# Kernel tuning notes

Hardware: AMD Instinct MI355X
Metric: run time of the kernel (lower is better)

The kernel has to match this reference:

```python
import jax, jax.numpy as jnp
import numpy as np

# ---- static config (matches init_kwargs and NSA hyperparams in source) ----
DIM = 512; HEADS = 8; DH = DIM // HEADS; DEPTH = 2
HH = 28; WW = 28; SEQ = HH * WW            # 784
WIN = 28 * 7                                # sliding window = 196
CBS = 28 * 14; CST = 28 * 7                 # compress block 392, stride 196
SBS = 28 * 14; NSEL = 1                     # selection block 392, top-1
NC = (SEQ - CBS) // CST + 1                 # 3 compressed blocks
NS = SEQ // SBS                             # 2 selection blocks
EPS = 1e-5
BATCH = 8


def _overlap_matrix():
    # fraction of each compressed block overlapping each selection block
    O = np.zeros((NC, NS), np.float32)
    for i in range(NC):
        a, b = i * CST, i * CST + CBS
        for j in range(NS):
            c, d = j * SBS, (j + 1) * SBS
            O[i, j] = max(0, min(b, d) - max(a, c)) / CBS
    return jnp.asarray(O)

OVERLAP = _overlap_matrix()  # [NC, NS]


def setup_inputs() -> dict:
    key = jax.random.key(0)
    ks = jax.random.split(key, 12)
    p = lambda i, shape, s=0.02: (jax.random.normal(ks[i], shape, jnp.float32) * s)
    return {
        "x": jax.random.normal(ks[0], (BATCH, DIM, HH, WW), jnp.float32),
        "pos_emb": jax.random.normal(ks[1], (SEQ,), jnp.float32),
        "attn_norm_g": jnp.ones((DEPTH, DIM), jnp.float32),
        "Wq": p(2, (DEPTH, DIM, HEADS * DH)),
        "Wk": p(3, (DEPTH, DIM, HEADS * DH)),
        "Wv": p(4, (DEPTH, DIM, HEADS * DH)),
        "Wo": p(5, (DEPTH, HEADS * DH, DIM)),
        "Wg": p(6, (DEPTH, DIM, HEADS * 3)),
        "ff_norm_g": jnp.ones((DEPTH, DIM), jnp.float32),
        "ff_norm_b": jnp.zeros((DEPTH, DIM), jnp.float32),
        "ff_w1": p(7, (DEPTH, 4 * DIM, DIM)),
        "ff_b1": jnp.zeros((DEPTH, 4 * DIM), jnp.float32),
        "ff_w2": p(8, (DEPTH, DIM, 4 * DIM)),
        "ff_b2": jnp.zeros((DEPTH, DIM), jnp.float32),
    }


def _sparse_attn(x, g, wq, wk, wv, wo, wg):
    # x: [b, n, d]  -- NSA: sliding window + compressed + top-k block selection
    b, n, d = x.shape
    xr = x * jax.lax.rsqrt(jnp.mean(x * x, -1, keepdims=True) + EPS) * g  # RMSNorm
    q = (xr @ wq).reshape(b, n, HEADS, DH)
    k = (xr @ wk).reshape(b, n, HEADS, DH)
    v = (xr @ wv).reshape(b, n, HEADS, DH)
    scale = DH ** -0.5

    # ---- compressed branch: mean-pool overlapping blocks ----
    ck = jnp.stack([k[:, i * CST:i * CST + CBS].mean(1) for i in range(NC)], 1)  # [b,NC,h,dh]
    cv = jnp.stack([v[:, i * CST:i * CST + CBS].mean(1) for i in range(NC)], 1)
    sc = jnp.einsum('bihd,bjhd->bhij', q, ck) * scale          # [b,h,n,NC]
    pc = jax.nn.softmax(sc, -1)
    out_c = jnp.einsum('bhij,bjhd->bihd', pc, cv)              # [b,n,h,dh]

    # ---- selection branch: importance -> top-k selection blocks -> fine attn ----
    imp = jnp.einsum('bhij,jk->bhik', pc, OVERLAP)             # [b,h,n,NS]
    _, sel = jax.lax.top_k(imp, NSEL)                          # [b,h,n,NSEL]
    selmask = jax.nn.one_hot(sel, NS, dtype=jnp.float32).sum(-2) > 0  # [b,h,n,NS]
    blk = jnp.arange(n) // SBS                                 # token -> selection block
    tokmask = selmask[..., blk]                                # [b,h,n,n]
    sf = jnp.einsum('bihd,bjhd->bhij', q, k) * scale           # full fine scores (shared)
    neg = jnp.finfo(sf.dtype).min
    ps = jax.nn.softmax(jnp.where(tokmask, sf, neg), -1)
    out_s = jnp.einsum('bhij,bjhd->bihd', ps, v)

    # ---- sliding window branch ----
    idx = jnp.arange(n)
    winmask = jnp.abs(idx[:, None] - idx[None, :]) < WIN       # [n,n]
    pw = jax.nn.softmax(jnp.where(winmask, sf, neg), -1)
    out_w = jnp.einsum('bhij,bjhd->bihd', pw, v)

    # ---- per-head learned gates over the 3 branches ----
    gates = jax.nn.sigmoid(xr @ wg).reshape(b, n, HEADS, 3)
    o = (gates[..., 0:1] * out_c + gates[..., 1:2] * out_s + gates[..., 2:3] * out_w)
    return o.reshape(b, n, HEADS * DH) @ wo


def _ff(x, g, bb, w1, b1, w2, b2):
    # x: [b,c,h,w]; LayerNorm over channel dim, then 1x1 conv -> GELU -> 1x1 conv
    mean = x.mean(1, keepdims=True)
    var = jnp.var(x, 1, keepdims=True)
    xn = (x - mean) / jnp.sqrt(var + EPS) * g[None, :, None, None] + bb[None, :, None, None]
    h1 = jax.nn.gelu(jnp.einsum('bchw,oc->bohw', xn, w1) + b1[None, :, None, None], approximate=False)
    return jnp.einsum('bchw,oc->bohw', h1, w2) + b2[None, :, None, None]


def reference(x, pos_emb, attn_norm_g, Wq, Wk, Wv, Wo, Wg,
              ff_norm_g, ff_norm_b, ff_w1, ff_b1, ff_w2, ff_b2):
    b, c, h, w = x.shape
    x = x + pos_emb[:h * w].reshape(1, 1, h, w)
    for l in range(DEPTH):
        s = x.reshape(b, c, h * w).transpose(0, 2, 1)          # b (h w) c
        s = _sparse_attn(s, attn_norm_g[l], Wq[l], Wk[l], Wv[l], Wo[l], Wg[l]) + s
        x = s.transpose(0, 2, 1).reshape(b, c, h, w)
        x = _ff(x, ff_norm_g[l], ff_norm_b[l], ff_w1[l], ff_b1[l], ff_w2[l], ff_b2[l]) + x
    return x
```

## Files before the change

kernel.cpp:

```cpp
#include <hip/hip_runtime.h>
#include <hip/hip_bf16.h>
#include <math.h>

#define B_      8
#define DIMC    512
#define SEQ_    784
#define HEADS_  8
#define DH_     64
#define NTOK    (B_*SEQ_)
#define QLD     1560
#define WIN_    196
#define CBS_    392
#define CST_    196
#define NC_     3
#define EPSF    1e-5f
#define FF_     2048
#define TQ_     28
#define MT_     98

typedef __hip_bfloat16 bf16_t;
typedef __attribute__((ext_vector_type(8))) short bf16x8;
typedef __attribute__((ext_vector_type(4))) float floatx4;
typedef __attribute__((ext_vector_type(4))) unsigned int uintx4;
typedef __attribute__((ext_vector_type(2))) unsigned int uintx2;

__device__ __forceinline__ float wsum(float x){
#pragma unroll
  for (int o = 32; o; o >>= 1) x += __shfl_xor(x, o, 64);
  return x;
}
__device__ __forceinline__ float geluf(float x){
  return 0.5f * x * (1.0f + erff(x * 0.70710678118654752f));
}
__device__ __forceinline__ float sigmoidf_(float x){
  return 1.0f / (1.0f + __expf(-x));
}

__global__ __launch_bounds__(256) void k_init(const float* __restrict__ xin,
                                              const float* __restrict__ pos,
                                              float* __restrict__ X){
  int idx = blockIdx.x * 256 + threadIdx.x;
  int c = idx & 511;
  int t = idx >> 9;
  int p = t % SEQ_;
  int b = t / SEQ_;
  float v = xin[((long)(b * DIMC + c)) * SEQ_ + p];
  X[idx] = v + pos[p];
}

__global__ __launch_bounds__(256) void k_final(const float* __restrict__ X,
                                               float* __restrict__ out){
  int idx = blockIdx.x * 256 + threadIdx.x;
  int p = idx % SEQ_;
  int t = idx / SEQ_;
  int c = t & 511;
  int b = t >> 9;
  out[idx] = X[((long)(b * SEQ_ + p)) * DIMC + c];
}

__global__ __launch_bounds__(256) void k_wconv1(const float* __restrict__ Wq,
                                                const float* __restrict__ Wk,
                                                const float* __restrict__ Wv,
                                                const float* __restrict__ Wg,
                                                bf16_t* __restrict__ Wb){
  int idx = blockIdx.x * 256 + threadIdx.x;
  int k = idx & 511;
  int t = idx >> 9;
  int n = t % QLD;
  int l = t / QLD;
  float v;
  if (n < 1536){
    int which = n >> 9;
    int nn = n & 511;
    const float* W = (which == 0) ? Wq : ((which == 1) ? Wk : Wv);
    v = W[((long)(l * 512 + k)) * 512 + nn];
  } else {
    v = Wg[((long)(l * 512 + k)) * 24 + (n - 1536)];
  }
  Wb[idx] = __float2bfloat16(v);
}

__global__ __launch_bounds__(256) void k_wconv2(const float* __restrict__ Wo,
                                                bf16_t* __restrict__ Wb){
  int idx = blockIdx.x * 256 + threadIdx.x;
  int k = idx & 511;
  int t = idx >> 9;
  int n = t & 511;
  int l = t >> 9;
  Wb[idx] = __float2bfloat16(Wo[((long)(l * 512 + k)) * 512 + n]);
}

__global__ __launch_bounds__(256) void k_cast(const float* __restrict__ src,
                                              bf16_t* __restrict__ dst){
  int idx = blockIdx.x * 256 + threadIdx.x;
  dst[idx] = __float2bfloat16(src[idx]);
}

__global__ __launch_bounds__(256) void k_zero(uintx4* __restrict__ p){
  p[blockIdx.x * 256 + threadIdx.x] = (uintx4){0u, 0u, 0u, 0u};
}

__global__ __launch_bounds__(256) void k_rms(const float* __restrict__ X,
                                             const float* __restrict__ g,
                                             bf16_t* __restrict__ XR){
  int tok = blockIdx.x;
  int tid = threadIdx.x;
  const float* xr = X + (long)tok * DIMC;
  float v0 = xr[tid], v1 = xr[tid + 256];
  float ss = v0 * v0 + v1 * v1;
  ss = wsum(ss);
  __shared__ float red[4];
  if ((tid & 63) == 0) red[tid >> 6] = ss;
  __syncthreads();
  float tot = red[0] + red[1] + red[2] + red[3];
  float r = rsqrtf(tot * (1.0f / DIMC) + EPSF);
  XR[(long)tok * DIMC + tid]       = __float2bfloat16(v0 * r * g[tid]);
  XR[(long)tok * DIMC + tid + 256] = __float2bfloat16(v1 * r * g[tid + 256]);
}

__global__ __launch_bounds__(256) void k_ln(const float* __restrict__ X,
                                            const float* __restrict__ g,
                                            const float* __restrict__ bb,
                                            bf16_t* __restrict__ XN){
  int tok = blockIdx.x;
  int tid = threadIdx.x;
  const float* xr = X + (long)tok * DIMC;
  float v0 = xr[tid], v1 = xr[tid + 256];
  float s = v0 + v1;
  float q = v0 * v0 + v1 * v1;
  s = wsum(s); q = wsum(q);
  __shared__ float r1[4], r2[4];
  if ((tid & 63) == 0){ r1[tid >> 6] = s; r2[tid >> 6] = q; }
  __syncthreads();
  float ts = r1[0] + r1[1] + r1[2] + r1[3];
  float tq = r2[0] + r2[1] + r2[2] + r2[3];
  float mean = ts * (1.0f / DIMC);
  float var  = tq * (1.0f / DIMC) - mean * mean;
  float rinv = rsqrtf(var + EPSF);
  XN[(long)tok * DIMC + tid]       = __float2bfloat16((v0 - mean) * rinv * g[tid]       + bb[tid]);
  XN[(long)tok * DIMC + tid + 256] = __float2bfloat16((v1 - mean) * rinv * g[tid + 256] + bb[tid + 256]);
}

template<int OUTBF, int ACT, int TN, int BK>
__global__ __launch_bounds__(256) void k_mgemm(const bf16_t* __restrict__ A,
                                               const bf16_t* __restrict__ Bm,
                                               float* Cf,
                                               bf16_t* Cb,
                                               const float* __restrict__ bias,
                                               const float* res,
                                               int M, int N, int K, int ldc, int ccol,
                                               bf16_t* VTo){
  constexpr int NTW = TN / 2;
  constexpr int NF  = TN / 32;
  constexpr int KS  = BK / 32;
  constexpr int AVN = (64 * BK) / 2048;
  constexpr int BVN = (TN * BK) / 2048;
  constexpr int RPB = BK / 8;
  constexpr int RST = 256 / RPB;

  int id = blockIdx.x;
  int xcd = id & 7;
  int j = id >> 3;
  int nt = j / 13;
  int mt = xcd * 13 + (j - nt * 13);
  if (mt >= MT_) return;
  int bm = mt * 64, bn = nt * TN;

  __shared__ bf16_t As[2][64][BK + 8];
  __shared__ bf16_t Bs[2][TN][BK + 8];
  int tid = threadIdx.x;
  int w = tid >> 6, lane = tid & 63;
  int wm = (w & 1) * 32, wn = (w >> 1) * NTW;
  int quad = lane >> 4, l16 = lane & 15;

  int vrow = tid / RPB;
  int vcol = (tid % RPB) * 8;
  const bf16_t* ap[AVN];
  const bf16_t* bp[BVN];
#pragma unroll
  for (int i = 0; i < AVN; i++)
    ap[i] = A + (long)(bm + vrow + i * RST) * K + vcol;
#pragma unroll
  for (int i = 0; i < BVN; i++){
    int r = bn + vrow + i * RST;
    if (r >= N) r = N - 1;
    bp[i] = Bm + (long)r * K + vcol;
  }

  floatx4 acc[2][NF];
#pragma unroll
  for (int i = 0; i < 2; i++)
#pragma unroll
    for (int jj = 0; jj < NF; jj++) acc[i][jj] = (floatx4)(0.0f);

  uintx4 aR[AVN], bR[BVN];
#pragma unroll
  for (int i = 0; i < AVN; i++) aR[i] = *(const uintx4*)ap[i];
#pragma unroll
  for (int i = 0; i < BVN; i++) bR[i] = *(const uintx4*)bp[i];

  int nch = K / BK;
  for (int ch = 0; ch < nch; ch++){
    int buf = ch & 1;
#pragma unroll
    for (int i = 0; i < AVN; i++) *(uintx4*)&As[buf][vrow + i * RST][vcol] = aR[i];
#pragma unroll
    for (int i = 0; i < BVN; i++) *(uintx4*)&Bs[buf][vrow + i * RST][vcol] = bR[i];
    __syncthreads();
    if (ch + 1 < nch){
      int ko = (ch + 1) * BK;
#pragma unroll
      for (int i = 0; i < AVN; i++) aR[i] = *(const uintx4*)(ap[i] + ko);
#pragma unroll
      for (int i = 0; i < BVN; i++) bR[i] = *(const uintx4*)(bp[i] + ko);
    }
#pragma unroll
    for (int ks = 0; ks < KS; ks++){
      bf16x8 a0 = *(bf16x8*)&As[buf][wm + l16][ks * 32 + quad * 8];
      bf16x8 a1 = *(bf16x8*)&As[buf][wm + 16 + l16][ks * 32 + quad * 8];
      bf16x8 bf[NF];
#pragma unroll
      for (int f = 0; f < NF; f++)
        bf[f] = *(bf16x8*)&Bs[buf][wn + f * 16 + l16][ks * 32 + quad * 8];
#pragma unroll
      for (int f = 0; f < NF; f++){
        acc[0][f] = __builtin_amdgcn_mfma_f32_16x16x32_bf16(a0, bf[f], acc[0][f], 0, 0, 0);
        acc[1][f] = __builtin_amdgcn_mfma_f32_16x16x32_bf16(a1, bf[f], acc[1][f], 0, 0, 0);
      }
    }
  }
#pragma unroll
  for (int tm = 0; tm < 2; tm++){
#pragma unroll
    for (int tn = 0; tn < NF; tn++){
      int ncol = bn + wn + tn * 16 + l16;
      if (ncol >= N) continue;
#pragma unroll
      for (int reg = 0; reg < 4; reg++){
        long mrow = bm + wm + tm * 16 + quad * 4 + reg;
        float v = acc[tm][tn][reg];
        if (bias) v += bias[ncol];
        if (ACT == 1) v = geluf(v);
        long off = mrow * (long)ldc + ccol + ncol;
        if (res) v += res[off];
        if (OUTBF){
          Cb[off] = __float2bfloat16(v);
          if (VTo && ncol >= 1024 && ncol < 1536){
            int bb2 = (int)(mrow / SEQ_);
            int tok = (int)(mrow - (long)bb2 * SEQ_);
            VTo[((long)(bb2 * 512 + (ncol - 1024))) * 800 + tok] = __float2bfloat16(v);
          }
        }
        else       Cf[off] = v;
      }
    }
  }
}

__global__ __launch_bounds__(512) void k_cpool(const bf16_t* __restrict__ qkvg,
                                               float* __restrict__ ck,
                                               float* __restrict__ cv){
  int bj = blockIdx.x;
  int j = bj % NC_;
  int b = bj / NC_;
  int tid = threadIdx.x;
  int seg = tid & 127;
  int rg  = tid >> 7;
  __shared__ float part[4][1024];
  const bf16_t* base = qkvg + ((long)b * SEQ_ + (long)j * CST_) * QLD + 512;
  float acc[8] = {0.f,0.f,0.f,0.f,0.f,0.f,0.f,0.f};
  for (int r = rg; r < CBS_; r += 4){
    uintx4 v = *(const uintx4*)(base + (long)r * QLD + seg * 8);
    bf16_t tmp[8]; *(uintx4*)tmp = v;
#pragma unroll
    for (int q = 0; q < 8; q++) acc[q] += __bfloat162float(tmp[q]);
  }
#pragma unroll
  for (int q = 0; q < 8; q++) part[rg][seg * 8 + q] = acc[q];
  __syncthreads();
  for (int c = tid; c < 1024; c += 512){
    float s = (part[0][c] + part[1][c]) + (part[2][c] + part[3][c]);
    s *= (1.0f / CBS_);
    if (c < 512) ck[bj * DIMC + c] = s;
    else         cv[bj * DIMC + (c - 512)] = s;
  }
}

__global__ __launch_bounds__(256) void k_attn(const bf16_t* __restrict__ qkvg,
                                              const float* __restrict__ ck,
                                              const float* __restrict__ cv,
                                              const bf16_t* __restrict__ vtg,
                                              bf16_t* __restrict__ oattn){
  int tid = threadIdx.x;
  int w = tid >> 6, lane = tid & 63;
  int quad = lane >> 4, l16 = lane & 15;
  int id = blockIdx.x;
  int xcd = id & 7;
  int j = id >> 3;
  int bh = xcd * 8 + (j / 28);
  int i0 = (j % 28) * TQ_;
  int h = bh & 7, b = bh >> 3;
  const float scale = 0.125f;

  __shared__ __align__(16) char smem[77040];
  bf16_t (*Qs)[72]    = (bf16_t(*)[72])(smem);
  bf16_t (*Ks0)[72]   = (bf16_t(*)[72])(smem + 4608);
  bf16_t (*Ks1)[72]   = (bf16_t(*)[72])(smem + 13824);
  bf16_t (*sbuf)[808] = (bf16_t(*)[808])(smem + 23040);
  float  (*outc_s)[64]= (float(*)[64])(smem + 68288);
  int*   sel_s = (int*)(smem + 75456);
  float* cw_s  = (float*)(smem + 75568);
  float* cs_s  = (float*)(smem + 75680);
  float* g1_s  = (float*)(smem + 75792);
  float* g2_s  = (float*)(smem + 75904);
  float (*red_s)[4][16] = (float(*)[4][16])(smem + 76016);

  const long rowBase = (long)b * SEQ_ * QLD + h * 64;

  if (tid < 224){
    int q = tid >> 3, seg = tid & 7;
    uintx4 qv = *(const uintx4*)(qkvg + rowBase + (long)(i0 + q) * QLD + seg * 8);
    *(uintx4*)&Qs[q][seg * 8] = qv;
  } else {
    int u = tid - 224;
    int r = 28 + (u >> 3), seg = u & 7;
    *(uintx4*)&Qs[r][seg * 8] = (uintx4){0u, 0u, 0u, 0u};
  }
  __syncthreads();

  int r0i = tid >> 3, s0i = tid & 7;
  int r1i = 32 + r0i;
  uintx4 kreg0 = *(const uintx4*)(qkvg + rowBase + (long)r0i * QLD + 512 + s0i * 8);
  uintx4 kreg1 = *(const uintx4*)(qkvg + rowBase + (long)r1i * QLD + 512 + s0i * 8);

  {
    const float* CKp = ck + (long)b * NC_ * DIMC + h * 64 + lane;
    const float* CVp = cv + (long)b * NC_ * DIMC + h * 64 + lane;
    float k0 = CKp[0], k1 = CKp[512], k2 = CKp[1024];
    float v0 = CVp[0], v1 = CVp[512], v2 = CVp[1024];
#pragma unroll
    for (int qp = 0; qp < 7; qp++){
      int qg = w * 7 + qp;
      float qd = __bfloat162float(Qs[qg][lane]);
      float s0 = wsum(qd * k0) * scale;
      float s1 = wsum(qd * k1) * scale;
      float s2 = wsum(qd * k2) * scale;
      float m3 = fmaxf(s0, fmaxf(s1, s2));
      float e0 = __expf(s0 - m3), e1 = __expf(s1 - m3), e2 = __expf(s2 - m3);
      float inv = 1.0f / (e0 + e1 + e2);
      const bf16_t* grow = qkvg + (long)(b * SEQ_ + i0 + qg) * QLD + 1536 + h * 3;
      float g0 = sigmoidf_(__bfloat162float(grow[0]));
      float g1v = sigmoidf_(__bfloat162float(grow[1]));
      float g2v = sigmoidf_(__bfloat162float(grow[2]));
      outc_s[qg][lane] = g0 * (e0 * v0 + e1 * v1 + e2 * v2) * inv;
      int selv = (s2 > s0) ? 1 : 0;
      if (lane == 0){ sel_s[qg] = selv; g1_s[qg] = g1v; g2_s[qg] = g2v; }
    }
  }

  bf16x8 a00 = *(bf16x8*)&Qs[l16][quad * 8];
  bf16x8 a01 = *(bf16x8*)&Qs[l16][32 + quad * 8];
  bf16x8 a10 = *(bf16x8*)&Qs[16 + l16][quad * 8];
  bf16x8 a11 = *(bf16x8*)&Qs[16 + l16][32 + quad * 8];

  __syncthreads();

  int sel0i = sel_s[l16];
  int sel1i = (l16 < 12) ? sel_s[16 + l16] : 0;
  bool sv0 = (sel0i != 0), sv1 = (sel1i != 0);
  int iq0 = i0 + l16, iq1 = i0 + 16 + l16;
  float sw0 = 0.f, ss0 = 0.f, sw1 = 0.f, ss1 = 0.f;

  for (int ch = 0; ch < 13; ch++){
    bf16_t (*Kb)[72] = (ch & 1) ? Ks1 : Ks0;
    *(uintx4*)&Kb[r0i][s0i * 8] = kreg0;
    *(uintx4*)&Kb[r1i][s0i * 8] = kreg1;
    __syncthreads();
    if (ch + 1 < 13){
      int c0n = (ch + 1) * 64;
      int t0 = c0n + r0i; if (t0 > 783) t0 = 783;
      int t1 = c0n + r1i; if (t1 > 783) t1 = 783;
      kreg0 = *(const uintx4*)(qkvg + rowBase + (long)t0 * QLD + 512 + s0i * 8);
      kreg1 = *(const uintx4*)(qkvg + rowBase + (long)t1 * QLD + 512 + s0i * 8);
    }
    bf16x8 k0 = *(bf16x8*)&Kb[w * 16 + l16][quad * 8];
    bf16x8 k1 = *(bf16x8*)&Kb[w * 16 + l16][32 + quad * 8];
    floatx4 d0 = (floatx4)(0.0f), d1 = (floatx4)(0.0f);
    d0 = __builtin_amdgcn_mfma_f32_16x16x32_bf16(k0, a00, d0, 0, 0, 0);
    d0 = __builtin_amdgcn_mfma_f32_16x16x32_bf16(k1, a01, d0, 0, 0, 0);
    d1 = __builtin_amdgcn_mfma_f32_16x16x32_bf16(k0, a10, d1, 0, 0, 0);
    d1 = __builtin_amdgcn_mfma_f32_16x16x32_bf16(k1, a11, d1, 0, 0, 0);
    int kb = ch * 64 + w * 16 + quad * 4;
    union { bf16_t hh[4]; uintx2 v; } p0, p1;
#pragma unroll
    for (int r = 0; r < 4; r++){
      int key = kb + r;
      float ex0 = __expf(d0[r] * scale);
      float ex1 = __expf(d1[r] * scale);
      bool valid = key < 784;
      if (valid && key >= iq0 - 195 && key <= iq0 + 195) sw0 += ex0;
      if (valid && ((key >= 392) == sv0))                ss0 += ex0;
      if (valid && key >= iq1 - 195 && key <= iq1 + 195) sw1 += ex1;
      if (valid && ((key >= 392) == sv1))                ss1 += ex1;
      p0.hh[r] = __float2bfloat16(ex0);
      p1.hh[r] = __float2bfloat16(ex1);
    }
    if (kb < 784){
      *(uintx2*)&sbuf[l16][kb] = p0.v;
      if (l16 < 12) *(uintx2*)&sbuf[16 + l16][kb] = p1.v;
    }
  }

  sw0 += __shfl_xor(sw0, 16, 64); sw0 += __shfl_xor(sw0, 32, 64);
  ss0 += __shfl_xor(ss0, 16, 64); ss0 += __shfl_xor(ss0, 32, 64);
  sw1 += __shfl_xor(sw1, 16, 64); sw1 += __shfl_xor(sw1, 32, 64);
  ss1 += __shfl_xor(ss1, 16, 64); ss1 += __shfl_xor(ss1, 32, 64);
  if (quad == 0){
    red_s[w][0][l16] = sw0; red_s[w][1][l16] = ss0;
    red_s[w][2][l16] = sw1; red_s[w][3][l16] = ss1;
  }
  __syncthreads();
  if (tid < 28){
    int q = tid, t = q >> 4, l = q & 15;
    float sw = 0.f, ss = 0.f;
#pragma unroll
    for (int wv = 0; wv < 4; wv++){ sw += red_s[wv][2 * t][l]; ss += red_s[wv][2 * t + 1][l]; }
    cw_s[q] = g2_s[q] / sw;
    cs_s[q] = g1_s[q] / ss;
  }
  __syncthreads();

  const bf16_t* vrow = vtg + ((long)(b * 512 + h * 64 + w * 16 + l16)) * 800 + quad * 8;
  bf16x8 bv = *(const bf16x8*)vrow;

  for (int t = tid; t < 2800; t += 256){
    int q = t / 100;
    int c0 = (t - q * 100) * 8;
    uintx4 ov;
    if (c0 >= 784){
      ov = (uintx4){0u, 0u, 0u, 0u};
    } else {
      union { bf16_t hh[8]; uintx4 v; } in, out;
      in.v = *(uintx4*)&sbuf[q][c0];
      int iq = i0 + q;
      float cwv = cw_s[q], csv = cs_s[q];
      float cse = ((c0 >= 392) == (sel_s[q] != 0)) ? csv : 0.0f;
#pragma unroll
      for (int jj = 0; jj < 8; jj++){
        int c = c0 + jj;
        float coef = cse;
        if (c >= iq - 195 && c <= iq + 195) coef += cwv;
        out.hh[jj] = __float2bfloat16(__bfloat162float(in.hh[jj]) * coef);
      }
      ov = out.v;
    }
    *(uintx4*)&sbuf[q][c0] = ov;
  }
  __syncthreads();

  floatx4 o0 = (floatx4)(0.0f), o1 = (floatx4)(0.0f);
#pragma unroll 5
  for (int st = 0; st < 25; st++){
    bf16x8 bcur = bv;
    if (st + 1 < 25) bv = *(const bf16x8*)(vrow + (st + 1) * 32);
    int kc = st * 32 + quad * 8;
    bf16x8 av0 = *(bf16x8*)&sbuf[l16][kc];
    bf16x8 av1 = *(bf16x8*)&sbuf[16 + l16][kc];
    o0 = __builtin_amdgcn_mfma_f32_16x16x32_bf16(av0, bcur, o0, 0, 0, 0);
    o1 = __builtin_amdgcn_mfma_f32_16x16x32_bf16(av1, bcur, o1, 0, 0, 0);
  }

  int d = w * 16 + l16;
#pragma unroll
  for (int reg = 0; reg < 4; reg++){
    int q = quad * 4 + reg;
    float o = o0[reg] + outc_s[q][d];
    oattn[((long)(b * SEQ_ + i0 + q)) * DIMC + h * 64 + d] = __float2bfloat16(o);
    int q2 = q + 16;
    if (q2 < 28){
      float o2 = o1[reg] + outc_s[q2][d];
      oattn[((long)(b * SEQ_ + i0 + q2)) * DIMC + h * 64 + d] = __float2bfloat16(o2);
    }
  }
}

extern "C" void kernel_launch(void* const* d_in, const int* in_sizes, int n_in,
                              void* d_out, int out_size, void* d_ws, size_t ws_size,
                              hipStream_t stream){
  const float* xin  = (const float*)d_in[0];
  const float* pos  = (const float*)d_in[1];
  const float* angm = (const float*)d_in[2];
  const float* Wq   = (const float*)d_in[3];
  const float* Wk   = (const float*)d_in[4];
  const float* Wv   = (const float*)d_in[5];
  const float* Wo   = (const float*)d_in[6];
  const float* Wg   = (const float*)d_in[7];
  const float* fng  = (const float*)d_in[8];
  const float* fnb  = (const float*)d_in[9];
  const float* fw1  = (const float*)d_in[10];
  const float* fb1  = (const float*)d_in[11];
  const float* fw2  = (const float*)d_in[12];
  const float* fb2  = (const float*)d_in[13];

  char* cw = (char*)d_ws;
  float* X = (float*)cw;             cw += (long)NTOK * 512 * 4;
  bf16_t* XRb = (bf16_t*)cw;         cw += (long)NTOK * 512 * 2;
  bf16_t* OAb = (bf16_t*)cw;         cw += (long)NTOK * 512 * 2;
  bf16_t* SH  = (bf16_t*)cw;         cw += (long)NTOK * FF_ * 2;
  float* CK = (float*)cw;            cw += (long)B_ * NC_ * DIMC * 4;
  float* CV = (float*)cw;            cw += (long)B_ * NC_ * DIMC * 4;
  bf16_t* Wqkvgb = (bf16_t*)cw;      cw += (long)2 * QLD * 512 * 2;
  bf16_t* WOb    = (bf16_t*)cw;      cw += (long)2 * 512 * 512 * 2;
  bf16_t* FW1b   = (bf16_t*)cw;      cw += (long)2 * FF_ * 512 * 2;
  bf16_t* FW2b   = (bf16_t*)cw;      cw += (long)2 * 512 * FF_ * 2;
  bf16_t* VTb    = (bf16_t*)cw;      cw += (long)B_ * 512 * 800 * 2;
  bf16_t* BUFb = SH;
  bf16_t* H1b  = SH;

  k_wconv1<<<(2 * QLD * 512) / 256, 256, 0, stream>>>(Wq, Wk, Wv, Wg, Wqkvgb);
  k_wconv2<<<(2 * 512 * 512) / 256, 256, 0, stream>>>(Wo, WOb);
  k_cast<<<(2 * FF_ * 512) / 256, 256, 0, stream>>>(fw1, FW1b);
  k_cast<<<(2 * 512 * FF_) / 256, 256, 0, stream>>>(fw2, FW2b);

  k_zero<<<1600, 256, 0, stream>>>((uintx4*)VTb);

  k_init<<<12544, 256, 0, stream>>>(xin, pos, X);

  for (int l = 0; l < 2; l++){
    k_rms<<<NTOK, 256, 0, stream>>>(X, angm + (long)l * DIMC, XRb);

    k_mgemm<1, 0, 128, 32><<<13 * 104, 256, 0, stream>>>(
        XRb, Wqkvgb + (long)l * QLD * 512, nullptr, BUFb, nullptr, nullptr,
        NTOK, QLD, 512, QLD, 0, VTb);

    k_cpool<<<B_ * NC_, 512, 0, stream>>>(BUFb, CK, CV);

    k_attn<<<8 * 8 * 28, 256, 0, stream>>>(BUFb, CK, CV, VTb, OAb);

    k_mgemm<0, 0, 64, 64><<<8 * 104, 256, 0, stream>>>(
        OAb, WOb + (long)l * 512 * 512, X, nullptr, nullptr, X,
        NTOK, 512, 512, 512, 0, nullptr);

    k_ln<<<NTOK, 256, 0, stream>>>(X, fng + (long)l * DIMC, fnb + (long)l * DIMC, XRb);

    k_mgemm<1, 1, 128, 32><<<16 * 104, 256, 0, stream>>>(
        XRb, FW1b + (long)l * FF_ * 512, nullptr, H1b, fb1 + (long)l * FF_, nullptr,
        NTOK, FF_, 512, FF_, 0, nullptr);
    k_mgemm<0, 0, 64, 64><<<8 * 104, 256, 0, stream>>>(
        H1b, FW2b + (long)l * 512 * FF_, X, nullptr, fb2 + (long)l * DIMC, X,
        NTOK, 512, FF_, 512, 0, nullptr);
  }

  k_final<<<12544, 256, 0, stream>>>(X, (float*)d_out);
}
```

Baseline: 651.1 us.

## Tile transposes via shared memory and fuse PV accumulation into score loop

Four transpose kernels (input/output layout change and weight conversion) now go through 32x33 shared-memory tiles, so both global reads and writes are coalesced. The attention kernel no longer stores the full 28x784 probability matrix in shared memory followed by a separate rescale pass and PV loop. It keeps separate window and selection probability tiles per 64-key chunk and accumulates P·V with MFMA inside the score loop, applying the per-query coefficients at the end. This cuts LDS use sharply, which may allow more blocks per CU, but it doubles the PV MFMAs and adds a barrier per chunk.

```diff
diff --git a/kernel.cpp b/kernel.cpp
--- a/kernel.cpp
+++ b/kernel.cpp
@@ -39,23 +39,48 @@
 __global__ __launch_bounds__(256) void k_init(const float* __restrict__ xin,
                                               const float* __restrict__ pos,
                                               float* __restrict__ X){
-  int idx = blockIdx.x * 256 + threadIdx.x;
-  int c = idx & 511;
-  int t = idx >> 9;
-  int p = t % SEQ_;
-  int b = t / SEQ_;
-  float v = xin[((long)(b * DIMC + c)) * SEQ_ + p];
-  X[idx] = v + pos[p];
+  __shared__ float tl[32][33];
+  int blk = blockIdx.x;
+  int ct = blk & 15;
+  int pt = (blk >> 4) % 25;
+  int b  = blk / (16 * 25);
+  int p0 = pt * 32, c0 = ct * 32;
+  int tx = threadIdx.x & 31, ty = threadIdx.x >> 5;
+#pragma unroll
+  for (int i = 0; i < 4; i++){
+    int p = p0 + tx;
+    if (p < SEQ_) tl[ty + i * 8][tx] = xin[((long)(b * DIMC + c0 + ty + i * 8)) * SEQ_ + p];
+  }
+  __syncthreads();
+#pragma unroll
+  for (int i = 0; i < 4; i++){
+    int p = p0 + ty + i * 8;
+    if (p < SEQ_)
+      X[((long)(b * SEQ_ + p)) * DIMC + c0 + tx] = tl[tx][ty + i * 8] + pos[p];
+  }
 }
 
 __global__ __launch_bounds__(256) void k_final(const float* __restrict__ X,
                                                float* __restrict__ out){
-  int idx = blockIdx.x * 256 + threadIdx.x;
-  int p = idx % SEQ_;
-  int t = idx / SEQ_;
-  int c = t & 511;
-  int b = t >> 9;
-  out[idx] = X[((long)(b * SEQ_ + p)) * DIMC + c];
+  __shared__ float tl[32][33];
+  int blk = blockIdx.x;
+  int ct = blk & 15;
+  int pt = (blk >> 4) % 25;
+  int b  = blk / (16 * 25);
+  int p0 = pt * 32, c0 = ct * 32;
+  int tx = threadIdx.x & 31, ty = threadIdx.x >> 5;
+#pragma unroll
+  for (int i = 0; i < 4; i++){
+    int p = p0 + ty + i * 8;
+    if (p < SEQ_) tl[ty + i * 8][tx] = X[((long)(b * SEQ_ + p)) * DIMC + c0 + tx];
+  }
+  __syncthreads();
+#pragma unroll
+  for (int i = 0; i < 4; i++){
+    int p = p0 + tx;
+    if (p < SEQ_)
+      out[((long)(b * DIMC + c0 + ty + i * 8)) * SEQ_ + p] = tl[tx][ty + i * 8];
+  }
 }
 
 __global__ __launch_bounds__(256) void k_wconv1(const float* __restrict__ Wq,
@@ -63,31 +88,51 @@
                                                 const float* __restrict__ Wv,
                                                 const float* __restrict__ Wg,
                                                 bf16_t* __restrict__ Wb){
-  int idx = blockIdx.x * 256 + threadIdx.x;
-  int k = idx & 511;
-  int t = idx >> 9;
-  int n = t % QLD;
-  int l = t / QLD;
-  float v;
-  if (n < 1536){
-    int which = n >> 9;
-    int nn = n & 511;
-    const float* W = (which == 0) ? Wq : ((which == 1) ? Wk : Wv);
-    v = W[((long)(l * 512 + k)) * 512 + nn];
-  } else {
-    v = Wg[((long)(l * 512 + k)) * 24 + (n - 1536)];
-  }
-  Wb[idx] = __float2bfloat16(v);
+  __shared__ float tl[32][33];
+  int blk = blockIdx.x;
+  int kt = blk & 15;
+  int ntf = (blk >> 4) % 49;
+  int l = blk / (16 * 49);
+  int n0 = ntf * 32, k0 = kt * 32;
+  int tx = threadIdx.x & 31, ty = threadIdx.x >> 5;
+#pragma unroll
+  for (int i = 0; i < 4; i++){
+    int n = n0 + tx, k = k0 + ty + i * 8;
+    float v = 0.0f;
+    if (n < 1536){
+      int which = n >> 9, nn = n & 511;
+      const float* W = (which == 0) ? Wq : ((which == 1) ? Wk : Wv);
+      v = W[((long)(l * 512 + k)) * 512 + nn];
+    } else if (n < QLD){
+      v = Wg[((long)(l * 512 + k)) * 24 + (n - 1536)];
+    }
+    tl[ty + i * 8][tx] = v;
+  }
+  __syncthreads();
+#pragma unroll
+  for (int i = 0; i < 4; i++){
+    int n = n0 + ty + i * 8, k = k0 + tx;
+    if (n < QLD)
+      Wb[((long)(l * QLD + n)) * 512 + k] = __float2bfloat16(tl[tx][ty + i * 8]);
+  }
 }
 
 __global__ __launch_bounds__(256) void k_wconv2(const float* __restrict__ Wo,
                                                 bf16_t* __restrict__ Wb){
-  int idx = blockIdx.x * 256 + threadIdx.x;
-  int k = idx & 511;
-  int t = idx >> 9;
-  int n = t & 511;
-  int l = t >> 9;
-  Wb[idx] = __float2bfloat16(Wo[((long)(l * 512 + k)) * 512 + n]);
+  __shared__ float tl[32][33];
+  int blk = blockIdx.x;
+  int kt = blk & 15;
+  int ntf = (blk >> 4) & 15;
+  int l = blk >> 8;
+  int n0 = ntf * 32, k0 = kt * 32;
+  int tx = threadIdx.x & 31, ty = threadIdx.x >> 5;
+#pragma unroll
+  for (int i = 0; i < 4; i++)
+    tl[ty + i * 8][tx] = Wo[((long)(l * 512 + k0 + ty + i * 8)) * 512 + n0 + tx];
+  __syncthreads();
+#pragma unroll
+  for (int i = 0; i < 4; i++)
+    Wb[((long)(l * 512 + n0 + ty + i * 8)) * 512 + k0 + tx] = __float2bfloat16(tl[tx][ty + i * 8]);
 }
 
 __global__ __launch_bounds__(256) void k_cast(const float* __restrict__ src,
@@ -302,18 +347,14 @@
   int h = bh & 7, b = bh >> 3;
   const float scale = 0.125f;
 
-  __shared__ __align__(16) char smem[77040];
-  bf16_t (*Qs)[72]    = (bf16_t(*)[72])(smem);
-  bf16_t (*Ks0)[72]   = (bf16_t(*)[72])(smem + 4608);
-  bf16_t (*Ks1)[72]   = (bf16_t(*)[72])(smem + 13824);
-  bf16_t (*sbuf)[808] = (bf16_t(*)[808])(smem + 23040);
-  float  (*outc_s)[64]= (float(*)[64])(smem + 68288);
-  int*   sel_s = (int*)(smem + 75456);
-  float* cw_s  = (float*)(smem + 75568);
-  float* cs_s  = (float*)(smem + 75680);
-  float* g1_s  = (float*)(smem + 75792);
-  float* g2_s  = (float*)(smem + 75904);
-  float (*red_s)[4][16] = (float(*)[4][16])(smem + 76016);
+  __shared__ bf16_t Qs[32][72];
+  __shared__ bf16_t Ks[2][64][72];
+  __shared__ bf16_t Wcw[2][32][72];
+  __shared__ bf16_t Wcs[2][32][72];
+  __shared__ float outc_s[28][64];
+  __shared__ int   sel_s[28];
+  __shared__ float cw_s[28], cs_s[28], g1_s[28], g2_s[28];
+  __shared__ float red_s[4][4][16];
 
   const long rowBase = (long)b * SEQ_ * QLD + h * 64;
 
@@ -325,6 +366,13 @@
     int u = tid - 224;
     int r = 28 + (u >> 3), seg = u & 7;
     *(uintx4*)&Qs[r][seg * 8] = (uintx4){0u, 0u, 0u, 0u};
+  }
+  for (int t = tid; t < 2 * 4 * 72; t += 256){
+    int bufi = t / (4 * 72);
+    int r = 28 + (t / 72) % 4;
+    int c = t % 72;
+    Wcw[bufi][r][c] = __float2bfloat16(0.0f);
+    Wcs[bufi][r][c] = __float2bfloat16(0.0f);
   }
   __syncthreads();
 
@@ -371,10 +419,15 @@
   int iq0 = i0 + l16, iq1 = i0 + 16 + l16;
   float sw0 = 0.f, ss0 = 0.f, sw1 = 0.f, ss1 = 0.f;
 
+  const bf16_t* vbase = vtg + ((long)(b * 512 + h * 64 + w * 16 + l16)) * 800;
+  floatx4 ow0 = (floatx4)(0.0f), ow1 = (floatx4)(0.0f);
+  floatx4 os0 = (floatx4)(0.0f), os1 = (floatx4)(0.0f);
+
   for (int ch = 0; ch < 13; ch++){
-    bf16_t (*Kb)[72] = (ch & 1) ? Ks1 : Ks0;
-    *(uintx4*)&Kb[r0i][s0i * 8] = kreg0;
-    *(uintx4*)&Kb[r1i][s0i * 8] = kreg1;
+    int buf = ch & 1;
+    int K0 = ch * 64;
+    *(uintx4*)&Ks[buf][r0i][s0i * 8] = kreg0;
+    *(uintx4*)&Ks[buf][r1i][s0i * 8] = kreg1;
     __syncthreads();
     if (ch + 1 < 13){
       int c0n = (ch + 1) * 64;
@@ -383,31 +436,54 @@
       kreg0 = *(const uintx4*)(qkvg + rowBase + (long)t0 * QLD + 512 + s0i * 8);
       kreg1 = *(const uintx4*)(qkvg + rowBase + (long)t1 * QLD + 512 + s0i * 8);
     }
-    bf16x8 k0 = *(bf16x8*)&Kb[w * 16 + l16][quad * 8];
-    bf16x8 k1 = *(bf16x8*)&Kb[w * 16 + l16][32 + quad * 8];
+    int tv0 = K0 + quad * 8;      if (tv0 > 792) tv0 = 792;
+    int tv1 = K0 + 32 + quad * 8; if (tv1 > 792) tv1 = 792;
+    bf16x8 bv0 = *(const bf16x8*)(vbase + tv0);
+    bf16x8 bv1 = *(const bf16x8*)(vbase + tv1);
+    bf16x8 k0 = *(bf16x8*)&Ks[buf][w * 16 + l16][quad * 8];
+    bf16x8 k1 = *(bf16x8*)&Ks[buf][w * 16 + l16][32 + quad * 8];
     floatx4 d0 = (floatx4)(0.0f), d1 = (floatx4)(0.0f);
     d0 = __builtin_amdgcn_mfma_f32_16x16x32_bf16(k0, a00, d0, 0, 0, 0);
     d0 = __builtin_amdgcn_mfma_f32_16x16x32_bf16(k1, a01, d0, 0, 0, 0);
     d1 = __builtin_amdgcn_mfma_f32_16x16x32_bf16(k0, a10, d1, 0, 0, 0);
     d1 = __builtin_amdgcn_mfma_f32_16x16x32_bf16(k1, a11, d1, 0, 0, 0);
-    int kb = ch * 64 + w * 16 + quad * 4;
-    union { bf16_t hh[4]; uintx2 v; } p0, p1;
+    int kb = K0 + w * 16 + quad * 4;
+    union { bf16_t hh[4]; uintx2 v; } pw0, ps0, pw1, ps1;
 #pragma unroll
     for (int r = 0; r < 4; r++){
       int key = kb + r;
       float ex0 = __expf(d0[r] * scale);
       float ex1 = __expf(d1[r] * scale);
       bool valid = key < 784;
-      if (valid && key >= iq0 - 195 && key <= iq0 + 195) sw0 += ex0;
-      if (valid && ((key >= 392) == sv0))                ss0 += ex0;
-      if (valid && key >= iq1 - 195 && key <= iq1 + 195) sw1 += ex1;
-      if (valid && ((key >= 392) == sv1))                ss1 += ex1;
-      p0.hh[r] = __float2bfloat16(ex0);
-      p1.hh[r] = __float2bfloat16(ex1);
-    }
-    if (kb < 784){
-      *(uintx2*)&sbuf[l16][kb] = p0.v;
-      if (l16 < 12) *(uintx2*)&sbuf[16 + l16][kb] = p1.v;
+      float vw0 = (valid && key >= iq0 - 195 && key <= iq0 + 195) ? ex0 : 0.0f;
+      float vs0 = (valid && ((key >= 392) == sv0))                ? ex0 : 0.0f;
+      float vw1 = (valid && key >= iq1 - 195 && key <= iq1 + 195) ? ex1 : 0.0f;
+      float vs1 = (valid && ((key >= 392) == sv1))                ? ex1 : 0.0f;
+      sw0 += vw0; ss0 += vs0; sw1 += vw1; ss1 += vs1;
+      pw0.hh[r] = __float2bfloat16(vw0);
+      ps0.hh[r] = __float2bfloat16(vs0);
+      pw1.hh[r] = __float2bfloat16(vw1);
+      ps1.hh[r] = __float2bfloat16(vs1);
+    }
+    int kloc = w * 16 + quad * 4;
+    *(uintx2*)&Wcw[buf][l16][kloc] = pw0.v;
+    *(uintx2*)&Wcs[buf][l16][kloc] = ps0.v;
+    if (l16 < 12){
+      *(uintx2*)&Wcw[buf][16 + l16][kloc] = pw1.v;
+      *(uintx2*)&Wcs[buf][16 + l16][kloc] = ps1.v;
+    }
+    __syncthreads();
+#pragma unroll
+    for (int ks = 0; ks < 2; ks++){
+      bf16x8 bv = ks ? bv1 : bv0;
+      bf16x8 aw0 = *(bf16x8*)&Wcw[buf][l16][ks * 32 + quad * 8];
+      bf16x8 aw1 = *(bf16x8*)&Wcw[buf][16 + l16][ks * 32 + quad * 8];
+      bf16x8 as0 = *(bf16x8*)&Wcs[buf][l16][ks * 32 + quad * 8];
+      bf16x8 as1 = *(bf16x8*)&Wcs[buf][16 + l16][ks * 32 + quad * 8];
+      ow0 = __builtin_amdgcn_mfma_f32_16x16x32_bf16(aw0, bv, ow0, 0, 0, 0);
+      ow1 = __builtin_amdgcn_mfma_f32_16x16x32_bf16(aw1, bv, ow1, 0, 0, 0);
+      os0 = __builtin_amdgcn_mfma_f32_16x16x32_bf16(as0, bv, os0, 0, 0, 0);
+      os1 = __builtin_amdgcn_mfma_f32_16x16x32_bf16(as1, bv, os1, 0, 0, 0);
     }
   }
 
@@ -430,55 +506,15 @@
   }
   __syncthreads();
 
-  const bf16_t* vrow = vtg + ((long)(b * 512 + h * 64 + w * 16 + l16)) * 800 + quad * 8;
-  bf16x8 bv = *(const bf16x8*)vrow;
-
-  for (int t = tid; t < 2800; t += 256){
-    int q = t / 100;
-    int c0 = (t - q * 100) * 8;
-    uintx4 ov;
-    if (c0 >= 784){
-      ov = (uintx4){0u, 0u, 0u, 0u};
-    } else {
-      union { bf16_t hh[8]; uintx4 v; } in, out;
-      in.v = *(uintx4*)&sbuf[q][c0];
-      int iq = i0 + q;
-      float cwv = cw_s[q], csv = cs_s[q];
-      float cse = ((c0 >= 392) == (sel_s[q] != 0)) ? csv : 0.0f;
-#pragma unroll
-      for (int jj = 0; jj < 8; jj++){
-        int c = c0 + jj;
-        float coef = cse;
-        if (c >= iq - 195 && c <= iq + 195) coef += cwv;
-        out.hh[jj] = __float2bfloat16(__bfloat162float(in.hh[jj]) * coef);
-      }
-      ov = out.v;
-    }
-    *(uintx4*)&sbuf[q][c0] = ov;
-  }
-  __syncthreads();
-
-  floatx4 o0 = (floatx4)(0.0f), o1 = (floatx4)(0.0f);
-#pragma unroll 5
-  for (int st = 0; st < 25; st++){
-    bf16x8 bcur = bv;
-    if (st + 1 < 25) bv = *(const bf16x8*)(vrow + (st + 1) * 32);
-    int kc = st * 32 + quad * 8;
-    bf16x8 av0 = *(bf16x8*)&sbuf[l16][kc];
-    bf16x8 av1 = *(bf16x8*)&sbuf[16 + l16][kc];
-    o0 = __builtin_amdgcn_mfma_f32_16x16x32_bf16(av0, bcur, o0, 0, 0, 0);
-    o1 = __builtin_amdgcn_mfma_f32_16x16x32_bf16(av1, bcur, o1, 0, 0, 0);
-  }
-
   int d = w * 16 + l16;
 #pragma unroll
   for (int reg = 0; reg < 4; reg++){
     int q = quad * 4 + reg;
-    float o = o0[reg] + outc_s[q][d];
+    float o = cw_s[q] * ow0[reg] + cs_s[q] * os0[reg] + outc_s[q][d];
     oattn[((long)(b * SEQ_ + i0 + q)) * DIMC + h * 64 + d] = __float2bfloat16(o);
     int q2 = q + 16;
     if (q2 < 28){
-      float o2 = o1[reg] + outc_s[q2][d];
+      float o2 = cw_s[q2] * ow1[reg] + cs_s[q2] * os1[reg] + outc_s[q2][d];
       oattn[((long)(b * SEQ_ + i0 + q2)) * DIMC + h * 64 + d] = __float2bfloat16(o2);
     }
   }
@@ -517,14 +553,14 @@
   bf16_t* BUFb = SH;
   bf16_t* H1b  = SH;
 
-  k_wconv1<<<(2 * QLD * 512) / 256, 256, 0, stream>>>(Wq, Wk, Wv, Wg, Wqkvgb);
-  k_wconv2<<<(2 * 512 * 512) / 256, 256, 0, stream>>>(Wo, WOb);
+  k_wconv1<<<2 * 49 * 16, 256, 0, stream>>>(Wq, Wk, Wv, Wg, Wqkvgb);
+  k_wconv2<<<2 * 16 * 16, 256, 0, stream>>>(Wo, WOb);
   k_cast<<<(2 * FF_ * 512) / 256, 256, 0, stream>>>(fw1, FW1b);
   k_cast<<<(2 * 512 * FF_) / 256, 256, 0, stream>>>(fw2, FW2b);
 
   k_zero<<<1600, 256, 0, stream>>>((uintx4*)VTb);
 
-  k_init<<<12544, 256, 0, stream>>>(xin, pos, X);
+  k_init<<<8 * 25 * 16, 256, 0, stream>>>(xin, pos, X);
 
   for (int l = 0; l < 2; l++){
     k_rms<<<NTOK, 256, 0, stream>>>(X, angm + (long)l * DIMC, XRb);
@@ -551,5 +587,5 @@
         NTOK, 512, FF_, 512, 0, nullptr);
   }
 
-  k_final<<<12544, 256, 0, stream>>>(X, (float*)d_out);
-}
+  k_final<<<8 * 25 * 16, 256, 0, stream>>>(X, (float*)d_out);
+}
```

Measured after the change: 575.3 us. 11.6% less time.
